# Kernel tuning notes

Measured on AMD Instinct MI355X. Metric: run time of the kernel, lower is better.

Reference implementation:

```python
import jax, jax.numpy as jnp
import numpy as np

ALPHA = 0.2
BETA = 1.0
TEMPERATURE = 0.05
EPS = 1e-8  # torch cosine_similarity eps


def setup_inputs() -> dict:
    key = jax.random.key(0)
    k1, k2 = jax.random.split(key)
    B, R, D = 4096, 18, 256  # rows, segment size (1 anchor + 1 pos + 16 negs), embed dim
    features = jax.random.normal(k1, (B * R, D), dtype=jnp.float32)
    scores = jax.random.normal(k2, (B * (R - 1),), dtype=jnp.float32)
    row_sizes = jnp.full((B,), R, dtype=jnp.int32)  # uniform ragged sizes
    logit_scale = jnp.array([1.0 / TEMPERATURE], dtype=jnp.float32)
    return {"features": features, "scores": scores, "row_sizes": row_sizes,
            "logit_scale": logit_scale}


def reference(features, scores, row_sizes, logit_scale):
    B = row_sizes.shape[0]
    R = features.shape[0] // B  # uniform segment size
    D = features.shape[1]
    f3 = features.reshape(B, R, D)
    anchor = f3[:, 0]          # [B, D]
    tgt = f3[:, 1:]            # [B, R-1, D]  (positive first, then negatives)

    # --- per-row cosine sims + log_softmax + KLDiv(batchmean) ---
    an = jnp.maximum(jnp.linalg.norm(anchor, axis=-1, keepdims=True), EPS)  # [B,1]
    tn = jnp.maximum(jnp.linalg.norm(tgt, axis=-1), EPS)                    # [B,R-1]
    cos = jnp.einsum('bd,bkd->bk', anchor, tgt) / (an * tn)                 # [B,R-1]
    emb_log = jax.nn.log_softmax(cos, axis=-1)                              # [B,R-1]
    ce = jax.nn.softmax(scores.reshape(B, R - 1), axis=-1)                  # [B,R-1]
    # torch KLDivLoss(reduction='batchmean') on a length-(R-1) vector divides by (R-1)
    kl = jnp.sum(ce * (jnp.log(ce) - emb_log), axis=-1) / (R - 1)           # [B]
    loss = jnp.mean(BETA * kl)

    # --- single InfoNCE over all rows: anchors vs [positives; all negatives] ---
    pos = f3[:, 1]                                   # [B, D]
    negs = f3[:, 2:].reshape(B * (R - 2), D)         # [B*(R-2), D]
    targets = jnp.concatenate([pos, negs], axis=0)   # [B*(R-1), D]
    logits = logit_scale[0] * (anchor @ targets.T)   # [B, B*(R-1)]
    labels = jnp.arange(B)
    # cross_entropy(logits, labels) with mean reduction
    infonce = jnp.mean(jax.nn.logsumexp(logits, axis=-1) - logits[labels, labels])

    return loss + ALPHA * infonce
```

## Files before the change

kernel.cpp:

```cpp
#include <hip/hip_runtime.h>
#include <math.h>

#define ALPHA 0.2f
#define BETA 1.0f
#define EPSV 1e-8f
#define LOG2E 1.4426950408889634f
#define LN2 0.6931471805599453f

#define BATCH 4096
#define RR 18
#define KT 17
#define DD 256
#define NTGT (BATCH*KT)

#define BMW 64
#define NWAVES 4
#define BMB (BMW*NWAVES)
#define MBLK (BATCH/BMB)
#define BN 64
#define NSPLIT 64
#define NSLOT (NSPLIT*2)
#define NSLICE (NTGT/NSPLIT)
#define NCHUNK (NSLICE/BN)
#define CHUNK_BYTES (BN*DD)

typedef int   i32x8  __attribute__((ext_vector_type(8)));
typedef float f32x16 __attribute__((ext_vector_type(16)));

__device__ inline void gl_lds16(const void* g, void* l){
  __builtin_amdgcn_global_load_lds(
      (const __attribute__((address_space(1))) unsigned int*)g,
      (__attribute__((address_space(3))) unsigned int*)l, 16, 0, 0);
}

__device__ inline int pk8(float a, float b, float c, float d){
  int p = __builtin_amdgcn_cvt_pk_fp8_f32(a, b, 0, false);
  return  __builtin_amdgcn_cvt_pk_fp8_f32(c, d, p, true);
}


__global__ __launch_bounds__(256) void prep_kernel(
    const float* __restrict__ feat, const float* __restrict__ scores,
    const float* __restrict__ lscale,
    unsigned char* __restrict__ abf8, unsigned char* __restrict__ tbf8,
    float* __restrict__ diag, float* __restrict__ klarr){
  __shared__ float csh[KT];
  int b = blockIdx.x, tid = threadIdx.x;
  int grp = tid >> 4, j = tid & 15;
  const float* fb = feat + (size_t)b * RR * DD;
  float s2 = lscale[0] * LOG2E;

  float4 a0 = ((const float4*)fb)[j*4+0];
  float4 a1 = ((const float4*)fb)[j*4+1];
  float4 a2 = ((const float4*)fb)[j*4+2];
  float4 a3 = ((const float4*)fb)[j*4+3];
  float asq = (a0.x*a0.x+a0.y*a0.y+a0.z*a0.z+a0.w*a0.w)
            + (a1.x*a1.x+a1.y*a1.y+a1.z*a1.z+a1.w*a1.w)
            + (a2.x*a2.x+a2.y*a2.y+a2.z*a2.z+a2.w*a2.w)
            + (a3.x*a3.x+a3.y*a3.y+a3.z*a3.z+a3.w*a3.w);
  #pragma unroll
  for (int off=1; off<16; off<<=1) asq += __shfl_xor(asq, off);
  float an = fmaxf(sqrtf(asq), EPSV);

  if (tid < 16){
    uint4 v = make_uint4(
      (unsigned)pk8(a0.x*s2,a0.y*s2,a0.z*s2,a0.w*s2),
      (unsigned)pk8(a1.x*s2,a1.y*s2,a1.z*s2,a1.w*s2),
      (unsigned)pk8(a2.x*s2,a2.y*s2,a2.z*s2,a2.w*s2),
      (unsigned)pk8(a3.x*s2,a3.y*s2,a3.z*s2,a3.w*s2));
    *(uint4*)(abf8 + (size_t)b*DD + j*16) = v;
  }

  for (int kr = grp+1; kr <= KT; kr += 16){
    const float4* tp = (const float4*)(fb + (size_t)kr*DD) + j*4;
    float4 t0=tp[0], t1=tp[1], t2=tp[2], t3=tp[3];
    int t  = b*KT + (kr-1);
    int c  = t >> 6, r = t & 63, mt = (r >> 5) & 1, m = r & 31;
    int ki = j >> 2, hf = (j >> 1) & 1, w = j & 1;
    uint4 v = make_uint4(
      (unsigned)pk8(t0.x,t0.y,t0.z,t0.w), (unsigned)pk8(t1.x,t1.y,t1.z,t1.w),
      (unsigned)pk8(t2.x,t2.y,t2.z,t2.w), (unsigned)pk8(t3.x,t3.y,t3.z,t3.w));
    *(uint4*)(tbf8 + (size_t)c*CHUNK_BYTES + (size_t)((ki*2+mt)*2+w)*1024
              + hf*512 + m*16) = v;
    float d = (a0.x*t0.x+a0.y*t0.y+a0.z*t0.z+a0.w*t0.w)
            + (a1.x*t1.x+a1.y*t1.y+a1.z*t1.z+a1.w*t1.w)
            + (a2.x*t2.x+a2.y*t2.y+a2.z*t2.z+a2.w*t2.w)
            + (a3.x*t3.x+a3.y*t3.y+a3.z*t3.z+a3.w*t3.w);
    float q = (t0.x*t0.x+t0.y*t0.y+t0.z*t0.z+t0.w*t0.w)
            + (t1.x*t1.x+t1.y*t1.y+t1.z*t1.z+t1.w*t1.w)
            + (t2.x*t2.x+t2.y*t2.y+t2.z*t2.z+t2.w*t2.w)
            + (t3.x*t3.x+t3.y*t3.y+t3.z*t3.z+t3.w*t3.w);
    #pragma unroll
    for (int off=1; off<16; off<<=1){ d += __shfl_xor(d,off); q += __shfl_xor(q,off); }
    if (j == 0){
      csh[kr-1] = d / (an * fmaxf(sqrtf(q), EPSV));
      if (kr == 1) diag[b] = d;
    }
  }
  __syncthreads();

  if (tid == 0){
    float cm = -INFINITY;
    #pragma unroll
    for (int i=0;i<KT;++i) cm = fmaxf(cm, csh[i]);
    float cs = 0.f;
    #pragma unroll
    for (int i=0;i<KT;++i) cs += __builtin_amdgcn_exp2f((csh[i]-cm)*LOG2E);
    float lse_c = cm + __logf(cs);

    const float* sb = scores + (size_t)b*KT;
    float sv[KT];
    #pragma unroll
    for (int i=0;i<KT;++i) sv[i] = sb[i];
    float sm = -INFINITY;
    #pragma unroll
    for (int i=0;i<KT;++i) sm = fmaxf(sm, sv[i]);
    float ss = 0.f;
    #pragma unroll
    for (int i=0;i<KT;++i) ss += __builtin_amdgcn_exp2f((sv[i]-sm)*LOG2E);
    float lse_s = sm + __logf(ss);

    float kl = 0.f;
    #pragma unroll
    for (int i=0;i<KT;++i){
      float lq = sv[i]  - lse_s;
      float lp = csh[i] - lse_c;
      kl += __builtin_amdgcn_exp2f(lq*LOG2E)*(lq - lp);
    }
    klarr[b] = kl * (1.0f/KT);
  }
}

__global__ __launch_bounds__(256,3) void gemm_lse_kernel(
    const unsigned char* __restrict__ abf8, const unsigned char* __restrict__ tbf8,
    float* __restrict__ part_m, float* __restrict__ part_s){
  __shared__ __align__(16) unsigned char Bs[2][CHUNK_BYTES];
  const int tid  = threadIdx.x;
  const int lane = tid & 63;
  const int wave = tid >> 6;
  const int mb   = blockIdx.y;
  const int ns   = blockIdx.x;
  const int l31  = lane & 31;
  const int half = lane >> 5;

  const char* gbase = (const char*)tbf8 + (size_t)(ns*NCHUNK)*CHUNK_BYTES;
  auto stage = [&](int ch){
    const char* g = gbase + (size_t)ch*CHUNK_BYTES;
    char* l = (char*)Bs[ch & 1];
    #pragma unroll
    for (int j=0;j<4;++j){
      int off = j*4096 + tid*16;
      gl_lds16(g + off, l + off);
    }
  };

  stage(0);

  i32x8 af[2][4];
  {
    const unsigned char* ab = abf8 + (size_t)(mb*BMB + wave*BMW)*DD;
    #pragma unroll
    for (int nt=0;nt<2;++nt)
      #pragma unroll
      for (int ki=0;ki<4;++ki){
        const unsigned char* p = ab + (size_t)(nt*32+l31)*DD + ki*64 + half*32;
        uint4 lo = *(const uint4*)p;
        uint4 hi = *(const uint4*)(p+16);
        af[nt][ki] = (i32x8){(int)lo.x,(int)lo.y,(int)lo.z,(int)lo.w,
                             (int)hi.x,(int)hi.y,(int)hi.z,(int)hi.w};
      }
  }

  float run_m[2] = {-INFINITY,-INFINITY};
  float run_s[2] = {0.f,0.f};

  for (int ch=0; ch<NCHUNK; ++ch){
    __syncthreads();
    if (ch+1 < NCHUNK) stage(ch+1);

    const unsigned char* frag = &Bs[ch & 1][0] + lane*16;

    f32x16 acc[2][2];
    #pragma unroll
    for (int mt=0;mt<2;++mt)
      #pragma unroll
      for (int nt=0;nt<2;++nt)
        acc[mt][nt] = (f32x16)(0.f);

    #pragma unroll
    for (int ki=0;ki<4;++ki){
      i32x8 tf[2];
      #pragma unroll
      for (int mt=0;mt<2;++mt){
        uint4 lo = *(const uint4*)(frag + (size_t)((ki*2+mt)*2+0)*1024);
        uint4 hi = *(const uint4*)(frag + (size_t)((ki*2+mt)*2+1)*1024);
        tf[mt] = (i32x8){(int)lo.x,(int)lo.y,(int)lo.z,(int)lo.w,
                         (int)hi.x,(int)hi.y,(int)hi.z,(int)hi.w};
      }
      acc[0][0] = __builtin_amdgcn_mfma_scale_f32_32x32x64_f8f6f4(
                      tf[0], af[0][ki], acc[0][0], 0,0, 0,127, 0,127);
      acc[0][1] = __builtin_amdgcn_mfma_scale_f32_32x32x64_f8f6f4(
                      tf[0], af[1][ki], acc[0][1], 0,0, 0,127, 0,127);
      acc[1][0] = __builtin_amdgcn_mfma_scale_f32_32x32x64_f8f6f4(
                      tf[1], af[0][ki], acc[1][0], 0,0, 0,127, 0,127);
      acc[1][1] = __builtin_amdgcn_mfma_scale_f32_32x32x64_f8f6f4(
                      tf[1], af[1][ki], acc[1][1], 0,0, 0,127, 0,127);
    }

    #pragma unroll
    for (int nt=0;nt<2;++nt){
      f32x16 t = __builtin_elementwise_max(acc[0][nt], acc[1][nt]);
      float m8[8];
      #pragma unroll
      for (int i=0;i<8;++i) m8[i] = fmaxf(t[i], t[i+8]);
      float m4a = fmaxf(m8[0],m8[1]), m4b = fmaxf(m8[2],m8[3]);
      float m4c = fmaxf(m8[4],m8[5]), m4d = fmaxf(m8[6],m8[7]);
      float mx = fmaxf(fmaxf(m4a,m4b), fmaxf(m4c,m4d));

      float s0=0.f, s1=0.f, s2=0.f, s3=0.f;
      #pragma unroll
      for (int r=0;r<16;r+=4){
        s0 += __builtin_amdgcn_exp2f(acc[0][nt][r  ]-mx) + __builtin_amdgcn_exp2f(acc[1][nt][r  ]-mx);
        s1 += __builtin_amdgcn_exp2f(acc[0][nt][r+1]-mx) + __builtin_amdgcn_exp2f(acc[1][nt][r+1]-mx);
        s2 += __builtin_amdgcn_exp2f(acc[0][nt][r+2]-mx) + __builtin_amdgcn_exp2f(acc[1][nt][r+2]-mx);
        s3 += __builtin_amdgcn_exp2f(acc[0][nt][r+3]-mx) + __builtin_amdgcn_exp2f(acc[1][nt][r+3]-mx);
      }
      float sh = (s0+s1)+(s2+s3);

      float nm = fmaxf(run_m[nt], mx);
      run_s[nt] = run_s[nt]*__builtin_amdgcn_exp2f(run_m[nt]-nm)
                + sh*__builtin_amdgcn_exp2f(mx-nm);
      run_m[nt] = nm;
    }
  }

  #pragma unroll
  for (int nt=0;nt<2;++nt){
    int gm = mb*BMB + wave*BMW + nt*32 + l31;
    int slot = ns*2 + half;
    part_m[(size_t)gm*NSLOT + slot] = run_m[nt];
    part_s[(size_t)gm*NSLOT + slot] = run_s[nt];
  }
}

__global__ __launch_bounds__(256) void combine_kernel(
    const float* __restrict__ part_m, const float* __restrict__ part_s,
    const float* __restrict__ diag, const float* __restrict__ lscale,
    float* __restrict__ infarr){
  int lane = threadIdx.x & 63, wave = threadIdx.x >> 6;
  int b = blockIdx.x*4 + wave;
  float s = lscale[0];
  const float* pm = part_m + (size_t)b*NSLOT;
  const float* ps = part_s + (size_t)b*NSLOT;
  float m0 = pm[lane], m1 = pm[lane+64];
  float v0 = ps[lane], v1 = ps[lane+64];
  float M = fmaxf(m0, m1);
  #pragma unroll
  for (int off=1; off<64; off<<=1) M = fmaxf(M, __shfl_xor(M, off));
  float S = v0*__builtin_amdgcn_exp2f(m0-M) + v1*__builtin_amdgcn_exp2f(m1-M);
  #pragma unroll
  for (int off=1; off<64; off<<=1) S += __shfl_xor(S, off);
  if (lane == 0)
    infarr[b] = (M + __log2f(S))*LN2 - s*diag[b];
}

__global__ __launch_bounds__(256) void final_kernel(
    const float* __restrict__ infarr, const float* __restrict__ klarr,
    float* __restrict__ out){
  __shared__ float shi[4], shk[4];
  int tid = threadIdx.x, lane = tid & 63, wave = tid >> 6;
  float inf = 0.f, kl = 0.f;
  for (int i = tid; i < BATCH; i += 256){ inf += infarr[i]; kl += klarr[i]; }
  #pragma unroll
  for (int off=1; off<64; off<<=1){
    inf += __shfl_xor(inf, off);
    kl  += __shfl_xor(kl,  off);
  }
  if (lane == 0){ shi[wave] = inf; shk[wave] = kl; }
  __syncthreads();
  if (tid == 0){
    float I = shi[0]+shi[1]+shi[2]+shi[3];
    float K = shk[0]+shk[1]+shk[2]+shk[3];
    out[0] = BETA*(K*(1.0f/BATCH)) + ALPHA*(I*(1.0f/BATCH));
  }
}

extern "C" void kernel_launch(void* const* d_in, const int* in_sizes, int n_in,
                              void* d_out, int out_size, void* d_ws, size_t ws_size,
                              hipStream_t stream){
  const float* feat   = (const float*)d_in[0];
  const float* scores = (const float*)d_in[1];
  const float* lscale = (const float*)d_in[3];

  float* ws     = (float*)d_ws;
  float* diag   = ws;
  float* klarr  = diag + BATCH;
  float* infarr = klarr + BATCH;
  float* part_m = infarr + BATCH;
  float* part_s = part_m + (size_t)BATCH*NSLOT;
  unsigned char* abf8 = (unsigned char*)(part_s + (size_t)BATCH*NSLOT);
  unsigned char* tbf8 = abf8 + (size_t)BATCH*DD;

  prep_kernel<<<BATCH, 256, 0, stream>>>(feat, scores, lscale, abf8, tbf8, diag, klarr);
  gemm_lse_kernel<<<dim3(NSPLIT, MBLK), 256, 0, stream>>>(abf8, tbf8, part_m, part_s);
  combine_kernel<<<BATCH/4, 256, 0, stream>>>(part_m, part_s, diag, lscale, infarr);
  final_kernel<<<1, 256, 0, stream>>>(infarr, klarr, (float*)d_out);
}
```

Measured before the change: 200.3 us.

## Use bit-trick exp2 in GEMM epilogue, widen N-split, merge halves before storing

The per-tile exp2 calls in the GEMM logsumexp epilogue become a Schraudolph-style approximation: one FMA plus a float-to-uint convert, with the row max folded into the constant. This targets transcendental-unit throughput. The max reduction now uses three-input max. The target split grows from 64 to 136 slices, which gives more blocks and shorter per-block loops. The two half-wave partials are merged in-register so the partial output holds one slot per split, and the combine kernel switches to a looped online-softmax merge. The KL tail in the prep kernel is spread across a wave instead of a single thread. The exp approximation adds a few percent relative error per term to the InfoNCE logsumexp, which may affect tolerance.

Result: slower. 204.7 us (+2.2%).

```diff
diff --git a/kernel.cpp b/kernel.cpp
--- a/kernel.cpp
+++ b/kernel.cpp
@@ -18,11 +18,14 @@
 #define BMB (BMW*NWAVES)
 #define MBLK (BATCH/BMB)
 #define BN 64
-#define NSPLIT 64
-#define NSLOT (NSPLIT*2)
+#define NSPLIT 136
+#define NSLOT NSPLIT
 #define NSLICE (NTGT/NSPLIT)
 #define NCHUNK (NSLICE/BN)
 #define CHUNK_BYTES (BN*DD)
+
+#define EXPA 8388608.0f
+#define EXPB 1064880320.0f
 
 typedef int   i32x8  __attribute__((ext_vector_type(8)));
 typedef float f32x16 __attribute__((ext_vector_type(16)));
@@ -36,6 +39,17 @@
 __device__ inline int pk8(float a, float b, float c, float d){
   int p = __builtin_amdgcn_cvt_pk_fp8_f32(a, b, 0, false);
   return  __builtin_amdgcn_cvt_pk_fp8_f32(c, d, p, true);
+}
+
+__device__ inline float fmax3(float a, float b, float c){
+  return fmaxf(fmaxf(a, b), c);
+}
+
+__device__ inline float fexp2u(float x, float kc){
+  float t = fmaf(x, EXPA, kc);
+  unsigned u;
+  asm("v_cvt_u32_f32 %0, %1" : "=v"(u) : "v"(t));
+  return __uint_as_float(u);
 }
 
 
@@ -99,35 +113,35 @@
   }
   __syncthreads();
 
-  if (tid == 0){
-    float cm = -INFINITY;
-    #pragma unroll
-    for (int i=0;i<KT;++i) cm = fmaxf(cm, csh[i]);
-    float cs = 0.f;
-    #pragma unroll
-    for (int i=0;i<KT;++i) cs += __builtin_amdgcn_exp2f((csh[i]-cm)*LOG2E);
+  if (tid < 64){
+    bool act = tid < KT;
+    float c  = act ? csh[tid] : -INFINITY;
+    float sv = act ? scores[(size_t)b*KT + tid] : -INFINITY;
+    float cm = c, sm = sv;
+    #pragma unroll
+    for (int off=1; off<64; off<<=1){
+      cm = fmaxf(cm, __shfl_xor(cm, off));
+      sm = fmaxf(sm, __shfl_xor(sm, off));
+    }
+    float ec = act ? __builtin_amdgcn_exp2f((c -cm)*LOG2E) : 0.f;
+    float es = act ? __builtin_amdgcn_exp2f((sv-sm)*LOG2E) : 0.f;
+    float cs = ec, ss = es;
+    #pragma unroll
+    for (int off=1; off<64; off<<=1){
+      cs += __shfl_xor(cs, off);
+      ss += __shfl_xor(ss, off);
+    }
     float lse_c = cm + __logf(cs);
-
-    const float* sb = scores + (size_t)b*KT;
-    float sv[KT];
-    #pragma unroll
-    for (int i=0;i<KT;++i) sv[i] = sb[i];
-    float sm = -INFINITY;
-    #pragma unroll
-    for (int i=0;i<KT;++i) sm = fmaxf(sm, sv[i]);
-    float ss = 0.f;
-    #pragma unroll
-    for (int i=0;i<KT;++i) ss += __builtin_amdgcn_exp2f((sv[i]-sm)*LOG2E);
     float lse_s = sm + __logf(ss);
-
-    float kl = 0.f;
-    #pragma unroll
-    for (int i=0;i<KT;++i){
-      float lq = sv[i]  - lse_s;
-      float lp = csh[i] - lse_c;
-      kl += __builtin_amdgcn_exp2f(lq*LOG2E)*(lq - lp);
-    }
-    klarr[b] = kl * (1.0f/KT);
+    float kt = 0.f;
+    if (act){
+      float lq = sv - lse_s;
+      float lp = c  - lse_c;
+      kt = __builtin_amdgcn_exp2f(lq*LOG2E)*(lq - lp);
+    }
+    #pragma unroll
+    for (int off=1; off<64; off<<=1) kt += __shfl_xor(kt, off);
+    if (tid == 0) klarr[b] = kt * (1.0f/KT);
   }
 }
 
@@ -210,20 +224,21 @@
     #pragma unroll
     for (int nt=0;nt<2;++nt){
       f32x16 t = __builtin_elementwise_max(acc[0][nt], acc[1][nt]);
-      float m8[8];
-      #pragma unroll
-      for (int i=0;i<8;++i) m8[i] = fmaxf(t[i], t[i+8]);
-      float m4a = fmaxf(m8[0],m8[1]), m4b = fmaxf(m8[2],m8[3]);
-      float m4c = fmaxf(m8[4],m8[5]), m4d = fmaxf(m8[6],m8[7]);
-      float mx = fmaxf(fmaxf(m4a,m4b), fmaxf(m4c,m4d));
-
+      float x0 = fmax3(t[0], t[1], t[2]);
+      float x1 = fmax3(t[3], t[4], t[5]);
+      float x2 = fmax3(t[6], t[7], t[8]);
+      float x3 = fmax3(t[9], t[10], t[11]);
+      float x4 = fmax3(t[12], t[13], t[14]);
+      float mx = fmaxf(fmax3(x0,x1,x2), fmax3(x3,x4,t[15]));
+
+      float kc = fmaf(mx, -EXPA, EXPB);
       float s0=0.f, s1=0.f, s2=0.f, s3=0.f;
       #pragma unroll
       for (int r=0;r<16;r+=4){
-        s0 += __builtin_amdgcn_exp2f(acc[0][nt][r  ]-mx) + __builtin_amdgcn_exp2f(acc[1][nt][r  ]-mx);
-        s1 += __builtin_amdgcn_exp2f(acc[0][nt][r+1]-mx) + __builtin_amdgcn_exp2f(acc[1][nt][r+1]-mx);
-        s2 += __builtin_amdgcn_exp2f(acc[0][nt][r+2]-mx) + __builtin_amdgcn_exp2f(acc[1][nt][r+2]-mx);
-        s3 += __builtin_amdgcn_exp2f(acc[0][nt][r+3]-mx) + __builtin_amdgcn_exp2f(acc[1][nt][r+3]-mx);
+        s0 += fexp2u(acc[0][nt][r  ],kc) + fexp2u(acc[1][nt][r  ],kc);
+        s1 += fexp2u(acc[0][nt][r+1],kc) + fexp2u(acc[1][nt][r+1],kc);
+        s2 += fexp2u(acc[0][nt][r+2],kc) + fexp2u(acc[1][nt][r+2],kc);
+        s3 += fexp2u(acc[0][nt][r+3],kc) + fexp2u(acc[1][nt][r+3],kc);
       }
       float sh = (s0+s1)+(s2+s3);
 
@@ -236,10 +251,16 @@
 
   #pragma unroll
   for (int nt=0;nt<2;++nt){
-    int gm = mb*BMB + wave*BMW + nt*32 + l31;
-    int slot = ns*2 + half;
-    part_m[(size_t)gm*NSLOT + slot] = run_m[nt];
-    part_s[(size_t)gm*NSLOT + slot] = run_s[nt];
+    float om = __shfl_xor(run_m[nt], 32);
+    float os = __shfl_xor(run_s[nt], 32);
+    float nm = fmaxf(run_m[nt], om);
+    float S  = run_s[nt]*__builtin_amdgcn_exp2f(run_m[nt]-nm)
+             + os*__builtin_amdgcn_exp2f(om-nm);
+    if (half == 0){
+      int gm = mb*BMB + wave*BMW + nt*32 + l31;
+      part_m[(size_t)gm*NSLOT + ns] = nm;
+      part_s[(size_t)gm*NSLOT + ns] = S;
+    }
   }
 }
 
@@ -252,16 +273,22 @@
   float s = lscale[0];
   const float* pm = part_m + (size_t)b*NSLOT;
   const float* ps = part_s + (size_t)b*NSLOT;
-  float m0 = pm[lane], m1 = pm[lane+64];
-  float v0 = ps[lane], v1 = ps[lane+64];
-  float M = fmaxf(m0, m1);
+  float m = -INFINITY, S = 0.f;
+  for (int i = lane; i < NSLOT; i += 64){
+    float pm_ = pm[i], ps_ = ps[i];
+    float nm = fmaxf(m, pm_);
+    S = S*__builtin_amdgcn_exp2f(m-nm) + ps_*__builtin_amdgcn_exp2f(pm_-nm);
+    m = nm;
+  }
   #pragma unroll
-  for (int off=1; off<64; off<<=1) M = fmaxf(M, __shfl_xor(M, off));
-  float S = v0*__builtin_amdgcn_exp2f(m0-M) + v1*__builtin_amdgcn_exp2f(m1-M);
-  #pragma unroll
-  for (int off=1; off<64; off<<=1) S += __shfl_xor(S, off);
+  for (int off=1; off<64; off<<=1){
+    float om = __shfl_xor(m, off), os = __shfl_xor(S, off);
+    float nm = fmaxf(m, om);
+    S = S*__builtin_amdgcn_exp2f(m-nm) + os*__builtin_amdgcn_exp2f(om-nm);
+    m = nm;
+  }
   if (lane == 0)
-    infarr[b] = (M + __log2f(S))*LN2 - s*diag[b];
+    infarr[b] = (m + __log2f(S))*LN2 - s*diag[b];
 }
 
 __global__ __launch_bounds__(256) void final_kernel(
```
